# Optimization experiments

Hardware: AMD Instinct MI355X
Metric: run time of the kernel (lower is better)

## Reference

```python
import jax, jax.numpy as jnp
import numpy as np

jax.config.update("jax_enable_x64", True)  # Q16.16 int64 fixed-point arithmetic requires 64-bit ints

F = 16                 # FixedPointConfig.COMPUTE_FRAC_BITS (Q16.16)
ONE = 1 << F

B, S, D_IN, D_OUT = 2, 2048, 4096, 4096


def setup_inputs() -> dict:
    key = jax.random.key(0)
    k1, k2 = jax.random.split(key)
    x = jax.random.normal(k1, (B, S, D_IN), dtype=jnp.float32)
    weight = jax.random.normal(k2, (D_OUT, D_IN), dtype=jnp.float32)
    return {"x": x, "weight": weight}


def _to_fixed(x):
    # to_fixed_point: float -> Q16.16 int64
    return jnp.round(x * ONE).astype(jnp.int64)


def _activation_quant_fixed(xf):
    # per-token 8-bit quant/dequant, all in Q16.16 integer arithmetic
    max_vals = jnp.max(jnp.abs(xf), axis=-1, keepdims=True)
    min_val = int(1e-5 * ONE)  # == 0 at frac_bits=16 (faithful to source)
    max_vals = jnp.maximum(max_vals, min_val)
    target_max = 127 << F
    # fixed_div(target_max, max_vals, F, F, F): (a << F) // b
    scale = (target_max << F) // max_vals
    # fixed_mul(x, scale, F, F, F): (a*b) >> F  (arithmetic shift == floor-div)
    x_scaled = (xf * scale) >> F
    x_clamped = jnp.clip(x_scaled, -(128 << F), 127 << F)
    # fixed_reciprocal(scale, F, F): (1 << 2F) // scale
    scale_inv = (1 << (2 * F)) // scale
    return (x_clamped * scale_inv) >> F


def reference(x, weight):
    # --- quantize_weights() ---
    wf = _to_fixed(weight)                                   # Q16.16
    mean_abs = jnp.sum(jnp.abs(wf)) // wf.size               # fixed_mean (Q16.16 scalar)
    # fixed_div(wf, mean_abs, F, F, 0) -> integer-valued; round+clamp to {-1,0,1}
    w_ternary = jnp.clip(wf // mean_abs, -1, 1).astype(jnp.int8)

    # --- forward ---
    xq = _activation_quant_fixed(_to_fixed(x))               # [B,S,D] Q16.16 int64
    xq2 = xq.reshape(-1, D_IN)
    # Ternary GEMM replacing the per-output-feature masked-sum loop.
    # |xq| <= 128<<16 ~ 8.4e6 and K=4096 => |acc| <= 3.4e10 < 2^53, so a
    acc = jnp.dot(xq2.astype(jnp.float64), w_ternary.astype(jnp.float64).T)
    out = jnp.round(acc).astype(jnp.int64)
    out = out.astype(jnp.int32).astype(jnp.int64)            # replicate torch .to(int32) wrap
    scale_inv = (1 << (2 * F)) // mean_abs                   # fixed_reciprocal of weight_scale
    out = (out * scale_inv) >> F                             # fixed_mul dequant/rescale
    out = out.reshape(B, S, D_OUT)
    return out.astype(jnp.float32) / ONE                     # from_fixed_point
```

## Files before the change

### kernel.cpp

```cpp
#include <hip/hip_runtime.h>
#include <stdint.h>

typedef int v4i  __attribute__((ext_vector_type(4)));
typedef int v16i __attribute__((ext_vector_type(16)));

static constexpr int Mdim = 4096;
static constexpr int Ndim = 4096;
static constexpr int Kdim = 4096;

static constexpr size_t TILE_BYTES  = 128u * 4096u;
static constexpr size_t OFF_BT      = 1u << 20;
static constexpr size_t OFF_A0      = 17u << 20;
static constexpr size_t PLANE_BYTES = 16u << 20;

__device__ __forceinline__ void gload16(const void* g, void* l) {
  __builtin_amdgcn_global_load_lds(
      (const __attribute__((address_space(1))) char*)g,
      (__attribute__((address_space(3))) char*)l, 16, 0, 0);
}

__global__ void k_wsum(const float* __restrict__ w, unsigned long long* __restrict__ ws) {
  int tid = blockIdx.x * blockDim.x + threadIdx.x;
  int stride = gridDim.x * blockDim.x;
  const float4* w4 = (const float4*)w;
  const int n4 = (Ndim * Kdim) / 4;
  unsigned long long s = 0;
  for (int i = tid; i < n4; i += stride) {
    float4 v = w4[i];
    int a = (int)rintf(v.x * 65536.f);
    int b = (int)rintf(v.y * 65536.f);
    int c = (int)rintf(v.z * 65536.f);
    int d = (int)rintf(v.w * 65536.f);
    unsigned u = (unsigned)(a < 0 ? -a : a) + (unsigned)(b < 0 ? -b : b)
               + (unsigned)(c < 0 ? -c : c) + (unsigned)(d < 0 ? -d : d);
    s += u;
  }
  #pragma unroll
  for (int off = 32; off > 0; off >>= 1) s += __shfl_down(s, off, 64);
  if ((threadIdx.x & 63) == 0) atomicAdd(ws, s);
}

__global__ void k_scalars(unsigned long long* ws) {
  unsigned long long s = ws[0];
  long long mean_abs = (long long)(s >> 24);
  if (mean_abs < 1) mean_abs = 1;
  long long siw = (long long)((1ULL << 32) / (unsigned long long)mean_abs);
  ((long long*)ws)[1] = siw;
  ((long long*)ws)[2] = mean_abs;
}

__global__ void k_tern(const float* __restrict__ w, const long long* __restrict__ scal,
                       int8_t* __restrict__ bt) {
  int t = blockIdx.x * 256 + threadIdx.x;
  int mean_abs = (int)scal[2];
  int nt = t >> 15;
  int kc = (t >> 7) & 255;
  int r  = t & 127;
  int row = nt * 128 + r;
  const float4* src = (const float4*)(w + (size_t)row * Kdim + kc * 16);
  int words[4];
  #pragma unroll
  for (int j = 0; j < 4; ++j) {
    float4 v = src[j];
    float e[4] = {v.x, v.y, v.z, v.w};
    int wrd = 0;
    #pragma unroll
    for (int q = 0; q < 4; ++q) {
      int f = (int)rintf(e[q] * 65536.f);
      int tv = (f >= mean_abs ? 1 : 0) - (f < 0 ? 1 : 0);
      wrd |= (tv & 0xff) << (8 * q);
    }
    words[j] = wrd;
  }
  *(int4*)(bt + (size_t)nt * TILE_BYTES + (size_t)kc * 2048 + (size_t)r * 16) =
      make_int4(words[0], words[1], words[2], words[3]);
}

__global__ void k_actq2(const float* __restrict__ x,
                        int8_t* __restrict__ a0, int8_t* __restrict__ a1, int8_t* __restrict__ a2) {
  int m   = blockIdx.x;
  int tid = threadIdx.x;
  const float4* src = (const float4*)(x + (size_t)m * Kdim + tid * 16);
  int xf[16];
  int mx = 0;
  #pragma unroll
  for (int j = 0; j < 4; ++j) {
    float4 v = src[j];
    float e[4] = {v.x, v.y, v.z, v.w};
    #pragma unroll
    for (int q = 0; q < 4; ++q) {
      int f = (int)rintf(e[q] * 65536.f);
      xf[j * 4 + q] = f;
      int af = f < 0 ? -f : f;
      mx = af > mx ? af : mx;
    }
  }
  #pragma unroll
  for (int off = 32; off > 0; off >>= 1) {
    int o = __shfl_down(mx, off, 64);
    mx = o > mx ? o : mx;
  }
  __shared__ int red[4];
  __shared__ long long sc[2];
  if ((tid & 63) == 0) red[tid >> 6] = mx;
  __syncthreads();
  if (tid == 0) {
    int m0 = red[0];
    m0 = red[1] > m0 ? red[1] : m0;
    m0 = red[2] > m0 ? red[2] : m0;
    m0 = red[3] > m0 ? red[3] : m0;
    if (m0 < 1) m0 = 1;
    long long scale = (long long)((127ULL << 32) / (unsigned long long)m0);
    long long sinv  = (long long)((1ULL << 32) / (unsigned long long)scale);
    sc[0] = scale; sc[1] = sinv;
  }
  __syncthreads();
  long long scale = sc[0];
  long long sinv  = sc[1];

  int w0[4], w1[4], w2[4];
  #pragma unroll
  for (int j = 0; j < 4; ++j) {
    int r0 = 0, r1 = 0, r2 = 0;
    #pragma unroll
    for (int q = 0; q < 4; ++q) {
      int v  = xf[j * 4 + q];
      int xs = (int)(((long long)v * scale) >> 16);
      xs = xs < -8388608 ? -8388608 : xs;
      xs = xs > 8323072 ? 8323072 : xs;
      int xq = (int)(((long long)xs * sinv) >> 16);
      int l0 = (int)(signed char)(xq & 0xff);
      int tt = (xq - l0) >> 8;
      int l1 = (int)(signed char)(tt & 0xff);
      int l2 = (tt - l1) >> 8;
      r0 |= (l0 & 0xff) << (8 * q);
      r1 |= (l1 & 0xff) << (8 * q);
      r2 |= (l2 & 0xff) << (8 * q);
    }
    w0[j] = r0; w1[j] = r1; w2[j] = r2;
  }
  size_t idx = (size_t)(m >> 7) * TILE_BYTES + (size_t)tid * 2048 + (size_t)(m & 127) * 16;
  *(int4*)(a0 + idx) = make_int4(w0[0], w0[1], w0[2], w0[3]);
  *(int4*)(a1 + idx) = make_int4(w1[0], w1[1], w1[2], w1[3]);
  *(int4*)(a2 + idx) = make_int4(w2[0], w2[1], w2[2], w2[3]);
}

__launch_bounds__(512)
__global__ void k_gemm(const int8_t* __restrict__ a0, const int8_t* __restrict__ a1,
                       const int8_t* __restrict__ a2, const int8_t* __restrict__ bt,
                       const long long* __restrict__ scal, float* __restrict__ out) {
  __shared__ __attribute__((aligned(16))) char lds[2][5][8192];
  int bx = (blockIdx.x & 7) * 64 + (blockIdx.x >> 3);
  int mt = bx >> 4;
  int nt = bx & 15;
  int tid  = threadIdx.x;
  int lane = tid & 63;
  int w    = tid >> 6;
  int wm   = w >> 2;
  int wn   = w & 3;

  const char* planes[5];
  planes[0] = (const char*)a0 + (size_t)mt * TILE_BYTES;
  planes[1] = (const char*)a1 + (size_t)mt * TILE_BYTES;
  planes[2] = (const char*)a2 + (size_t)mt * TILE_BYTES;
  planes[3] = (const char*)bt + (size_t)(2 * nt) * TILE_BYTES;
  planes[4] = (const char*)bt + (size_t)(2 * nt + 1) * TILE_BYTES;

  v16i acc[2][2][3] = {};

  auto STAGE = [&](int buf, int kt) {
    #pragma unroll
    for (int p = 0; p < 5; ++p)
      gload16(planes[p] + (size_t)kt * 8192 + (size_t)tid * 16, &lds[buf][p][tid * 16]);
  };

  auto COMPUTE = [&](int buf) {
    #pragma unroll
    for (int ks = 0; ks < 2; ++ks) {
      const int koff = (ks * 2 + (lane >> 5)) * 2048;
      v4i afrag[2][3], bfrag[2];
      #pragma unroll
      for (int mf = 0; mf < 2; ++mf)
        #pragma unroll
        for (int p = 0; p < 3; ++p)
          afrag[mf][p] = *(const v4i*)&lds[buf][p][koff + (wm * 64 + mf * 32 + (lane & 31)) * 16];
      #pragma unroll
      for (int nj = 0; nj < 2; ++nj) {
        int col = wn * 64 + nj * 32 + (lane & 31);
        bfrag[nj] = *(const v4i*)&lds[buf][3 + (col >> 7)][koff + (col & 127) * 16];
      }
      __builtin_amdgcn_s_setprio(1);
      #pragma unroll
      for (int mf = 0; mf < 2; ++mf)
        #pragma unroll
        for (int nj = 0; nj < 2; ++nj)
          #pragma unroll
          for (int p = 0; p < 3; ++p)
            acc[mf][nj][p] = __builtin_amdgcn_mfma_i32_32x32x32_i8(
                afrag[mf][p], bfrag[nj], acc[mf][nj][p], 0, 0, 0);
      __builtin_amdgcn_s_setprio(0);
    }
  };

  const int NT = Kdim / 64;
  STAGE(0, 0);
  __syncthreads();
  for (int t = 0; t < NT; ++t) {
    int cur = t & 1;
    if (t + 1 < NT) STAGE(cur ^ 1, t + 1);
    COMPUTE(cur);
    __syncthreads();
  }

  long long siw = scal[1];
  #pragma unroll
  for (int mf = 0; mf < 2; ++mf) {
    int m0 = mt * 128 + wm * 64 + mf * 32;
    #pragma unroll
    for (int nj = 0; nj < 2; ++nj) {
      int n0 = nt * 256 + wn * 64 + nj * 32;
      #pragma unroll
      for (int rg = 0; rg < 16; ++rg) {
        unsigned u = (unsigned)acc[mf][nj][0][rg]
                   + ((unsigned)acc[mf][nj][1][rg] << 8)
                   + ((unsigned)acc[mf][nj][2][rg] << 16);
        long long v = ((long long)(int)u * siw) >> 16;
        int row = (rg & 3) + 8 * (rg >> 2) + 4 * (lane >> 5);
        int col = lane & 31;
        out[(size_t)(m0 + row) * Ndim + (n0 + col)] = (float)v * (1.f / 65536.f);
      }
    }
  }
}

extern "C" void kernel_launch(void* const* d_in, const int* in_sizes, int n_in,
                              void* d_out, int out_size, void* d_ws, size_t ws_size,
                              hipStream_t stream) {
  const float* x = (const float*)d_in[0];
  const float* w = (const float*)d_in[1];
  float* out = (float*)d_out;
  char* ws = (char*)d_ws;

  unsigned long long* scal = (unsigned long long*)ws;
  int8_t* bt = (int8_t*)(ws + OFF_BT);
  int8_t* a0 = (int8_t*)(ws + OFF_A0);
  int8_t* a1 = a0 + PLANE_BYTES;
  int8_t* a2 = a1 + PLANE_BYTES;

  hipMemsetAsync(ws, 0, 64, stream);
  k_wsum<<<1024, 256, 0, stream>>>(w, scal);
  k_scalars<<<1, 1, 0, stream>>>(scal);
  k_tern<<<4096, 256, 0, stream>>>(w, (const long long*)scal, bt);
  k_actq2<<<4096, 256, 0, stream>>>(x, a0, a1, a2);
  k_gemm<<<512, 512, 0, stream>>>(a0, a1, a2, bt, (const long long*)scal, out);
}
```

Measured before the change: 430.1 us.

## Load GEMM fragments directly from global, fold scalar kernel, batch rows in prep kernels

The GEMM no longer stages A and B tiles through LDS with double buffering and barriers. Each wave now reads its MFMA fragments straight from global memory into registers. The separate scalar kernel is removed, and mean_abs and its reciprocal are recomputed inside the ternarize and GEMM kernels. The ternarize and activation-quant kernels each process four rows per block, and the GEMM block-to-tile mapping is changed to group M tiles per XCD. Dropping LDS staging removes barrier and LDS traffic, but it relies on L2/L1 for operand reuse across waves and loses load/compute overlap.

```diff
diff --git a/kernel.cpp b/kernel.cpp
--- a/kernel.cpp
+++ b/kernel.cpp
@@ -12,12 +12,6 @@
 static constexpr size_t OFF_BT      = 1u << 20;
 static constexpr size_t OFF_A0      = 17u << 20;
 static constexpr size_t PLANE_BYTES = 16u << 20;
-
-__device__ __forceinline__ void gload16(const void* g, void* l) {
-  __builtin_amdgcn_global_load_lds(
-      (const __attribute__((address_space(1))) char*)g,
-      (__attribute__((address_space(3))) char*)l, 16, 0, 0);
-}
 
 __global__ void k_wsum(const float* __restrict__ w, unsigned long long* __restrict__ ws) {
   int tid = blockIdx.x * blockDim.x + threadIdx.x;
@@ -40,155 +34,167 @@
   if ((threadIdx.x & 63) == 0) atomicAdd(ws, s);
 }
 
-__global__ void k_scalars(unsigned long long* ws) {
-  unsigned long long s = ws[0];
-  long long mean_abs = (long long)(s >> 24);
-  if (mean_abs < 1) mean_abs = 1;
-  long long siw = (long long)((1ULL << 32) / (unsigned long long)mean_abs);
-  ((long long*)ws)[1] = siw;
-  ((long long*)ws)[2] = mean_abs;
-}
-
-__global__ void k_tern(const float* __restrict__ w, const long long* __restrict__ scal,
+__global__ void k_tern(const float* __restrict__ w, const unsigned long long* __restrict__ ws,
                        int8_t* __restrict__ bt) {
-  int t = blockIdx.x * 256 + threadIdx.x;
-  int mean_abs = (int)scal[2];
-  int nt = t >> 15;
-  int kc = (t >> 7) & 255;
-  int r  = t & 127;
-  int row = nt * 128 + r;
-  const float4* src = (const float4*)(w + (size_t)row * Kdim + kc * 16);
-  int words[4];
+  long long ma = (long long)(ws[0] >> 24);
+  int mean_abs = ma < 1 ? 1 : (int)ma;
+  int row0 = blockIdx.x * 4;
+  int rr = threadIdx.x >> 6;
+  int c6 = threadIdx.x & 63;
+  int row = row0 + rr;
+  int8_t* dst = bt + (size_t)(row >> 7) * TILE_BYTES + (size_t)(row & 127) * 16;
+  const float* srow = w + (size_t)row * Kdim;
   #pragma unroll
   for (int j = 0; j < 4; ++j) {
-    float4 v = src[j];
-    float e[4] = {v.x, v.y, v.z, v.w};
-    int wrd = 0;
-    #pragma unroll
-    for (int q = 0; q < 4; ++q) {
-      int f = (int)rintf(e[q] * 65536.f);
-      int tv = (f >= mean_abs ? 1 : 0) - (f < 0 ? 1 : 0);
-      wrd |= (tv & 0xff) << (8 * q);
-    }
-    words[j] = wrd;
-  }
-  *(int4*)(bt + (size_t)nt * TILE_BYTES + (size_t)kc * 2048 + (size_t)r * 16) =
-      make_int4(words[0], words[1], words[2], words[3]);
-}
-
-__global__ void k_actq2(const float* __restrict__ x,
+    int kc = j * 64 + c6;
+    const float4* src = (const float4*)(srow + kc * 16);
+    int words[4];
+    #pragma unroll
+    for (int jj = 0; jj < 4; ++jj) {
+      float4 v = src[jj];
+      float e[4] = {v.x, v.y, v.z, v.w};
+      int wrd = 0;
+      #pragma unroll
+      for (int q = 0; q < 4; ++q) {
+        int f = (int)rintf(e[q] * 65536.f);
+        int tv = (f >= mean_abs ? 1 : 0) - (f < 0 ? 1 : 0);
+        wrd |= (tv & 0xff) << (8 * q);
+      }
+      words[jj] = wrd;
+    }
+    *(int4*)(dst + (size_t)kc * 2048) = make_int4(words[0], words[1], words[2], words[3]);
+  }
+}
+
+__global__ void k_actq4(const float* __restrict__ x,
                         int8_t* __restrict__ a0, int8_t* __restrict__ a1, int8_t* __restrict__ a2) {
-  int m   = blockIdx.x;
+  int m0 = blockIdx.x * 4;
   int tid = threadIdx.x;
-  const float4* src = (const float4*)(x + (size_t)m * Kdim + tid * 16);
-  int xf[16];
-  int mx = 0;
-  #pragma unroll
-  for (int j = 0; j < 4; ++j) {
-    float4 v = src[j];
-    float e[4] = {v.x, v.y, v.z, v.w};
-    #pragma unroll
-    for (int q = 0; q < 4; ++q) {
-      int f = (int)rintf(e[q] * 65536.f);
-      xf[j * 4 + q] = f;
-      int af = f < 0 ? -f : f;
-      mx = af > mx ? af : mx;
-    }
-  }
-  #pragma unroll
-  for (int off = 32; off > 0; off >>= 1) {
-    int o = __shfl_down(mx, off, 64);
-    mx = o > mx ? o : mx;
-  }
   __shared__ int red[4];
   __shared__ long long sc[2];
-  if ((tid & 63) == 0) red[tid >> 6] = mx;
-  __syncthreads();
-  if (tid == 0) {
-    int m0 = red[0];
-    m0 = red[1] > m0 ? red[1] : m0;
-    m0 = red[2] > m0 ? red[2] : m0;
-    m0 = red[3] > m0 ? red[3] : m0;
-    if (m0 < 1) m0 = 1;
-    long long scale = (long long)((127ULL << 32) / (unsigned long long)m0);
-    long long sinv  = (long long)((1ULL << 32) / (unsigned long long)scale);
-    sc[0] = scale; sc[1] = sinv;
-  }
-  __syncthreads();
-  long long scale = sc[0];
-  long long sinv  = sc[1];
-
-  int w0[4], w1[4], w2[4];
-  #pragma unroll
-  for (int j = 0; j < 4; ++j) {
-    int r0 = 0, r1 = 0, r2 = 0;
-    #pragma unroll
-    for (int q = 0; q < 4; ++q) {
-      int v  = xf[j * 4 + q];
-      int xs = (int)(((long long)v * scale) >> 16);
-      xs = xs < -8388608 ? -8388608 : xs;
-      xs = xs > 8323072 ? 8323072 : xs;
-      int xq = (int)(((long long)xs * sinv) >> 16);
-      int l0 = (int)(signed char)(xq & 0xff);
-      int tt = (xq - l0) >> 8;
-      int l1 = (int)(signed char)(tt & 0xff);
-      int l2 = (tt - l1) >> 8;
-      r0 |= (l0 & 0xff) << (8 * q);
-      r1 |= (l1 & 0xff) << (8 * q);
-      r2 |= (l2 & 0xff) << (8 * q);
-    }
-    w0[j] = r0; w1[j] = r1; w2[j] = r2;
-  }
-  size_t idx = (size_t)(m >> 7) * TILE_BYTES + (size_t)tid * 2048 + (size_t)(m & 127) * 16;
-  *(int4*)(a0 + idx) = make_int4(w0[0], w0[1], w0[2], w0[3]);
-  *(int4*)(a1 + idx) = make_int4(w1[0], w1[1], w1[2], w1[3]);
-  *(int4*)(a2 + idx) = make_int4(w2[0], w2[1], w2[2], w2[3]);
+  for (int rr = 0; rr < 4; ++rr) {
+    int m = m0 + rr;
+    const float4* src = (const float4*)(x + (size_t)m * Kdim + tid * 16);
+    int xf[16];
+    int mx = 0;
+    #pragma unroll
+    for (int j = 0; j < 4; ++j) {
+      float4 v = src[j];
+      float e[4] = {v.x, v.y, v.z, v.w};
+      #pragma unroll
+      for (int q = 0; q < 4; ++q) {
+        int f = (int)rintf(e[q] * 65536.f);
+        xf[j * 4 + q] = f;
+        int af = f < 0 ? -f : f;
+        mx = af > mx ? af : mx;
+      }
+    }
+    #pragma unroll
+    for (int off = 32; off > 0; off >>= 1) {
+      int o = __shfl_down(mx, off, 64);
+      mx = o > mx ? o : mx;
+    }
+    if ((tid & 63) == 0) red[tid >> 6] = mx;
+    __syncthreads();
+    if (tid == 0) {
+      int mm = red[0];
+      mm = red[1] > mm ? red[1] : mm;
+      mm = red[2] > mm ? red[2] : mm;
+      mm = red[3] > mm ? red[3] : mm;
+      if (mm < 1) mm = 1;
+      long long scale = (long long)((127ULL << 32) / (unsigned long long)mm);
+      long long sinv  = (long long)((1ULL << 32) / (unsigned long long)scale);
+      sc[0] = scale; sc[1] = sinv;
+    }
+    __syncthreads();
+    long long scale = sc[0];
+    long long sinv  = sc[1];
+    int w0[4], w1[4], w2[4];
+    #pragma unroll
+    for (int j = 0; j < 4; ++j) {
+      int r0 = 0, r1 = 0, r2 = 0;
+      #pragma unroll
+      for (int q = 0; q < 4; ++q) {
+        int v  = xf[j * 4 + q];
+        int xs = (int)(((long long)v * scale) >> 16);
+        xs = xs < -8388608 ? -8388608 : xs;
+        xs = xs > 8323072 ? 8323072 : xs;
+        int xq = (int)(((long long)xs * sinv) >> 16);
+        int l0 = (int)(signed char)(xq & 0xff);
+        int tt = (xq - l0) >> 8;
+        int l1 = (int)(signed char)(tt & 0xff);
+        int l2 = (tt - l1) >> 8;
+        r0 |= (l0 & 0xff) << (8 * q);
+        r1 |= (l1 & 0xff) << (8 * q);
+        r2 |= (l2 & 0xff) << (8 * q);
+      }
+      w0[j] = r0; w1[j] = r1; w2[j] = r2;
+    }
+    size_t idx = (size_t)(m >> 7) * TILE_BYTES + (size_t)tid * 2048 + (size_t)(m & 127) * 16;
+    *(int4*)(a0 + idx) = make_int4(w0[0], w0[1], w0[2], w0[3]);
+    *(int4*)(a1 + idx) = make_int4(w1[0], w1[1], w1[2], w1[3]);
+    *(int4*)(a2 + idx) = make_int4(w2[0], w2[1], w2[2], w2[3]);
+    __syncthreads();
+  }
 }
 
 __launch_bounds__(512)
 __global__ void k_gemm(const int8_t* __restrict__ a0, const int8_t* __restrict__ a1,
                        const int8_t* __restrict__ a2, const int8_t* __restrict__ bt,
-                       const long long* __restrict__ scal, float* __restrict__ out) {
-  __shared__ __attribute__((aligned(16))) char lds[2][5][8192];
-  int bx = (blockIdx.x & 7) * 64 + (blockIdx.x >> 3);
-  int mt = bx >> 4;
-  int nt = bx & 15;
+                       const unsigned long long* __restrict__ ws, float* __restrict__ out) {
+  int b = blockIdx.x;
+  int xcd = b & 7;
+  int rb  = b >> 3;
+  int nt  = rb & 15;
+  int mt  = xcd * 4 + (rb >> 4);
   int tid  = threadIdx.x;
   int lane = tid & 63;
   int w    = tid >> 6;
   int wm   = w >> 2;
   int wn   = w & 3;
-
-  const char* planes[5];
-  planes[0] = (const char*)a0 + (size_t)mt * TILE_BYTES;
-  planes[1] = (const char*)a1 + (size_t)mt * TILE_BYTES;
-  planes[2] = (const char*)a2 + (size_t)mt * TILE_BYTES;
-  planes[3] = (const char*)bt + (size_t)(2 * nt) * TILE_BYTES;
-  planes[4] = (const char*)bt + (size_t)(2 * nt + 1) * TILE_BYTES;
+  int l31  = lane & 31;
+  int hi   = lane >> 5;
+
+  const char* A[3] = { (const char*)a0 + (size_t)mt * TILE_BYTES,
+                       (const char*)a1 + (size_t)mt * TILE_BYTES,
+                       (const char*)a2 + (size_t)mt * TILE_BYTES };
+  int offA[2][2];
+  #pragma unroll
+  for (int ks = 0; ks < 2; ++ks)
+    #pragma unroll
+    for (int mf = 0; mf < 2; ++mf)
+      offA[ks][mf] = (ks * 2 + hi) * 2048 + (wm * 64 + mf * 32 + l31) * 16;
+
+  const char* Bb[2];
+  int offB[2][2];
+  #pragma unroll
+  for (int nj = 0; nj < 2; ++nj) {
+    int col = wn * 64 + nj * 32 + l31;
+    Bb[nj] = (const char*)bt + (size_t)(2 * nt + (col >> 7)) * TILE_BYTES;
+    #pragma unroll
+    for (int ks = 0; ks < 2; ++ks)
+      offB[ks][nj] = (ks * 2 + hi) * 2048 + (col & 127) * 16;
+  }
 
   v16i acc[2][2][3] = {};
 
-  auto STAGE = [&](int buf, int kt) {
-    #pragma unroll
-    for (int p = 0; p < 5; ++p)
-      gload16(planes[p] + (size_t)kt * 8192 + (size_t)tid * 16, &lds[buf][p][tid * 16]);
-  };
-
-  auto COMPUTE = [&](int buf) {
-    #pragma unroll
-    for (int ks = 0; ks < 2; ++ks) {
-      const int koff = (ks * 2 + (lane >> 5)) * 2048;
-      v4i afrag[2][3], bfrag[2];
+  for (int t = 0; t < Kdim / 64; ++t) {
+    const size_t tb = (size_t)t * 8192;
+    v4i bf[2][2], af[2][2][3];
+    #pragma unroll
+    for (int ks = 0; ks < 2; ++ks)
+      #pragma unroll
+      for (int nj = 0; nj < 2; ++nj)
+        bf[ks][nj] = *(const v4i*)(Bb[nj] + tb + offB[ks][nj]);
+    #pragma unroll
+    for (int ks = 0; ks < 2; ++ks)
       #pragma unroll
       for (int mf = 0; mf < 2; ++mf)
         #pragma unroll
         for (int p = 0; p < 3; ++p)
-          afrag[mf][p] = *(const v4i*)&lds[buf][p][koff + (wm * 64 + mf * 32 + (lane & 31)) * 16];
-      #pragma unroll
-      for (int nj = 0; nj < 2; ++nj) {
-        int col = wn * 64 + nj * 32 + (lane & 31);
-        bfrag[nj] = *(const v4i*)&lds[buf][3 + (col >> 7)][koff + (col & 127) * 16];
-      }
+          af[ks][mf][p] = *(const v4i*)(A[p] + tb + offA[ks][mf]);
+    #pragma unroll
+    for (int ks = 0; ks < 2; ++ks) {
       __builtin_amdgcn_s_setprio(1);
       #pragma unroll
       for (int mf = 0; mf < 2; ++mf)
@@ -197,22 +203,14 @@
           #pragma unroll
           for (int p = 0; p < 3; ++p)
             acc[mf][nj][p] = __builtin_amdgcn_mfma_i32_32x32x32_i8(
-                afrag[mf][p], bfrag[nj], acc[mf][nj][p], 0, 0, 0);
+                af[ks][mf][p], bf[ks][nj], acc[mf][nj][p], 0, 0, 0);
       __builtin_amdgcn_s_setprio(0);
     }
-  };
-
-  const int NT = Kdim / 64;
-  STAGE(0, 0);
-  __syncthreads();
-  for (int t = 0; t < NT; ++t) {
-    int cur = t & 1;
-    if (t + 1 < NT) STAGE(cur ^ 1, t + 1);
-    COMPUTE(cur);
-    __syncthreads();
-  }
-
-  long long siw = scal[1];
+  }
+
+  long long ma = (long long)(ws[0] >> 24);
+  if (ma < 1) ma = 1;
+  long long siw = (long long)((1ULL << 32) / (unsigned long long)ma);
   #pragma unroll
   for (int mf = 0; mf < 2; ++mf) {
     int m0 = mt * 128 + wm * 64 + mf * 32;
@@ -225,8 +223,8 @@
                    + ((unsigned)acc[mf][nj][1][rg] << 8)
                    + ((unsigned)acc[mf][nj][2][rg] << 16);
         long long v = ((long long)(int)u * siw) >> 16;
-        int row = (rg & 3) + 8 * (rg >> 2) + 4 * (lane >> 5);
-        int col = lane & 31;
+        int row = (rg & 3) + 8 * (rg >> 2) + 4 * hi;
+        int col = l31;
         out[(size_t)(m0 + row) * Ndim + (n0 + col)] = (float)v * (1.f / 65536.f);
       }
     }
@@ -249,8 +247,7 @@
 
   hipMemsetAsync(ws, 0, 64, stream);
   k_wsum<<<1024, 256, 0, stream>>>(w, scal);
-  k_scalars<<<1, 1, 0, stream>>>(scal);
-  k_tern<<<4096, 256, 0, stream>>>(w, (const long long*)scal, bt);
-  k_actq2<<<4096, 256, 0, stream>>>(x, a0, a1, a2);
-  k_gemm<<<512, 512, 0, stream>>>(a0, a1, a2, bt, (const long long*)scal, out);
-}
+  k_tern<<<1024, 256, 0, stream>>>(w, scal, bt);
+  k_actq4<<<1024, 256, 0, stream>>>(x, a0, a1, a2);
+  k_gemm<<<512, 512, 0, stream>>>(a0, a1, a2, bt, scal, out);
+}
```

New measurement: 813.7 us. 89.2% more time.
